# Kernel optimization log

Hardware: AMD Instinct MI355X
Metric: run time of the kernel (lower is better)

Reference implementation:

```python
import jax, jax.numpy as jnp
import numpy as np
from jax import lax

HFACTOR = 0.5


def setup_inputs() -> dict:
    key = jax.random.key(0)
    ks = jax.random.split(key, 10)
    B, T, D, K, C = 256, 128, 768, 74, 128
    feats = jax.random.normal(ks[0], (B, T, D), jnp.float32)
    attention_mask = jnp.ones((B, T), jnp.int32)
    labels = jax.random.randint(ks[1], (B, T), 0, K)
    cache = jax.random.normal(ks[2], (C, 128, K), jnp.float32)
    W1 = jax.random.normal(ks[3], (D, K), jnp.float32) * 0.02
    b1 = jnp.zeros((K,), jnp.float32)
    W2 = jax.random.normal(ks[4], (K, K), jnp.float32) * 0.1
    b2 = jnp.zeros((K,), jnp.float32)
    start_trans = jax.random.normal(ks[5], (K,), jnp.float32) * 0.1
    end_trans = jax.random.normal(ks[6], (K,), jnp.float32) * 0.1
    transitions = jax.random.normal(ks[7], (K, K), jnp.float32) * 0.1
    return dict(feats=feats, attention_mask=attention_mask, labels=labels,
                cache=cache, W1=W1, b1=b1, W2=W2, b2=b2,
                start_trans=start_trans, end_trans=end_trans,
                transitions=transitions)


def _crf_normalizer(em, mask, start, end, trans):
    # em: [T,B,K], mask: [T,B] bool -> log partition per batch [B]
    score0 = start[None, :] + em[0]
    def step(score, inp):
        e, m = inp
        nxt = jax.nn.logsumexp(score[:, :, None] + trans[None] + e[:, None, :], axis=1)
        return jnp.where(m[:, None], nxt, score), None
    score, _ = lax.scan(step, score0, (em[1:], mask[1:]))
    return jax.nn.logsumexp(score + end[None, :], axis=1)


def _crf_score(em, tags, mask, start, end, trans):
    # em: [T,B,K], tags: [T,B], mask: [T,B] -> gold path score [B]
    T, B, K = em.shape
    b = jnp.arange(B)
    score0 = start[tags[0]] + em[0, b, tags[0]]
    maskf = mask.astype(em.dtype)
    def step(carry, inp):
        score, prev = carry
        e, t, m = inp
        score = score + (trans[prev, t] + e[b, t]) * m
        return (score, t), None
    (score, _), _ = lax.scan(step, (score0, tags[0]), (em[1:], tags[1:], maskf[1:]))
    seq_ends = jnp.sum(mask.astype(jnp.int32), axis=0) - 1  # [B]
    last = tags[seq_ends, b]
    return score + end[last]


def _viterbi(em, mask, start, end, trans):
    # em: [T,B,K], mask: [T,B] bool -> best tag sequence [B,T]
    T, B, K = em.shape
    b = jnp.arange(B)
    score0 = start[None, :] + em[0]
    def fwd(score, inp):
        e, m = inp
        br = score[:, :, None] + trans[None]          # [B,K_prev,K_cur]
        idx = jnp.argmax(br, axis=1)                  # [B,K]
        nxt = jnp.max(br, axis=1) + e
        return jnp.where(m[:, None], nxt, score), idx
    score, hist = lax.scan(fwd, score0, (em[1:], mask[1:]))  # hist: [T-1,B,K]
    best_last = jnp.argmax(score + end[None, :], axis=1)     # [B]
    def back(cur, inp):
        h, m = inp                                    # h: [B,K], m: [B]
        cur_t = jnp.where(m, h[b, cur], best_last)
        return cur_t, cur_t
    _, tags_rev = lax.scan(back, best_last, (hist[::-1], mask[1:][::-1]))
    tags = jnp.concatenate([tags_rev[::-1], best_last[None]], axis=0)  # [T,B]
    return tags.T


def reference(feats, attention_mask, labels, cache, W1, b1, W2, b2,
              start_trans, end_trans, transitions):
    T = feats.shape[1]
    logits = feats @ W1 + b1                                   # [B,T,K]
    c = cache[:, :T]                                           # [C,T,K]
    sim = jnp.einsum('pjk,qjk->pq', logits, c)                 # [B,C]
    p = jax.nn.softmax(sim, axis=1)
    h = jnp.einsum('ij,jkl->ikl', p, c)                        # [B,T,K]
    new_logits = (logits + h * HFACTOR) @ W2 + b2              # [B,T,K]
    em = jnp.transpose(new_logits, (1, 0, 2))                  # [T,B,K]
    mask_t = attention_mask.T.astype(bool)                     # [T,B]
    prob = _viterbi(em, mask_t, start_trans, end_trans, transitions)
    num = _crf_score(em, labels.T, mask_t, start_trans, end_trans, transitions)
    den = _crf_normalizer(em, mask_t, start_trans, end_trans, transitions)
    loss = -jnp.mean(num - den)                                # torchcrf reduction='mean', negated
    return (prob, loss)
```

## Files before the change

### kernel.cpp

```cpp
#include <hip/hip_runtime.h>

#define B_ 256
#define T_ 128
#define D_ 768
#define K_ 74
#define C_ 128
#define TK_ 9472
#define BT_ 32768
#define EMS_ 18944

#define LGKM_BARRIER() do { \
    asm volatile("s_waitcnt lgkmcnt(0)" ::: "memory"); \
    __builtin_amdgcn_s_barrier(); \
    __builtin_amdgcn_sched_barrier(0); \
} while (0)

__global__ void pad_weights(const float* __restrict__ W1, const float* __restrict__ W2,
                            float* __restrict__ W1q, float* __restrict__ W2q)
{
    int idx = blockIdx.x * 256 + threadIdx.x;
    if (idx < 4 * 768 * 20) {
        int nq = idx / (768 * 20); int rem = idx - nq * (768 * 20);
        int k = rem / 20, j = rem - k * 20;
        int c = nq * 19 + j;
        W1q[idx] = (j < 19 && c < 74) ? W1[k * 74 + c] : 0.f;
    }
    if (idx < 4 * 74 * 20) {
        int nq = idx / (74 * 20); int rem = idx - nq * (74 * 20);
        int k = rem / 20, j = rem - k * 20;
        int c = nq * 19 + j;
        W2q[idx] = (j < 19 && c < 74) ? W2[k * 74 + c] : 0.f;
    }
}

__global__ __launch_bounds__(256) void gemm_logits(const float* __restrict__ feats,
    const float* __restrict__ W1q, const float* __restrict__ b1, float* __restrict__ logits)
{
    int orig = blockIdx.x;
    int vb = (orig & 7) * 64 + (orig >> 3);
    int rb = vb >> 2, nq = vb & 3;
    int tid = threadIdx.x;
    int r = rb * 256 + tid;
    int c0 = nq * 19;
    const float* frow = feats + (size_t)r * 768;
    const float* wq = W1q + nq * (768 * 20);
    float acc[20];
    #pragma unroll
    for (int j = 0; j < 20; ++j) acc[j] = 0.f;

    for (int k0 = 0; k0 < 768; k0 += 16) {
        float4 a[4];
        #pragma unroll
        for (int q = 0; q < 4; ++q) a[q] = *(const float4*)(frow + k0 + 4 * q);
        #pragma unroll
        for (int u = 0; u < 16; ++u) {
            float av = ((const float*)a)[u];
            const float* wr = wq + (k0 + u) * 20;
            #pragma unroll
            for (int j = 0; j < 20; ++j) acc[j] += av * wr[j];
        }
    }
    #pragma unroll
    for (int j = 0; j < 19; ++j) {
        int c = c0 + j;
        if (c < 74) logits[(size_t)r * 74 + c] = acc[j] + b1[c];
    }
}

__global__ __launch_bounds__(256) void sim_partial(const float* __restrict__ logits,
    const float* __restrict__ cache, float* __restrict__ part)
{
    __shared__ float As[74][68];
    __shared__ float Bs[74][68];
    int tid = threadIdx.x;
    int tx = tid & 15, ty = tid >> 4;
    int bid = blockIdx.x;
    int jc = bid >> 3;
    int mt = (bid >> 1) & 3;
    int nt = bid & 1;
    int p0 = mt * 64, q0 = nt * 64;
    float acc[4][4] = {};
    for (int jj = 0; jj < 4; ++jj) {
        int j = jc * 4 + jj;
        for (int it = 0; it < 19; ++it) {
            int lin = it * 256 + tid;
            if (lin < 64 * 74) {
                int r = lin / 74, ik = lin - r * 74;
                As[ik][r] = logits[(p0 + r) * TK_ + j * 74 + ik];
                Bs[ik][r] = cache[(q0 + r) * TK_ + j * 74 + ik];
            }
        }
        __syncthreads();
        for (int ik = 0; ik < 74; ++ik) {
            float4 a = *(const float4*)&As[ik][4 * tx];
            float4 b = *(const float4*)&Bs[ik][4 * ty];
            const float* ap = (const float*)&a;
            const float* bp = (const float*)&b;
            #pragma unroll
            for (int i = 0; i < 4; ++i)
                #pragma unroll
                for (int q = 0; q < 4; ++q) acc[i][q] += ap[i] * bp[q];
        }
        __syncthreads();
    }
    #pragma unroll
    for (int i = 0; i < 4; ++i)
        #pragma unroll
        for (int q = 0; q < 4; ++q)
            part[jc * (B_ * C_) + (p0 + 4 * tx + i) * C_ + q0 + 4 * ty + q] = acc[i][q];
}

__global__ void sim_reduce(const float* __restrict__ part, float* __restrict__ sim)
{
    int idx = blockIdx.x * 256 + threadIdx.x;
    float s = 0.f;
    for (int jc = 0; jc < 32; ++jc) s += part[jc * (B_ * C_) + idx];
    sim[idx] = s;
}

__global__ void softmax128(const float* __restrict__ sim, float* __restrict__ p)
{
    __shared__ float red[128];
    int q = threadIdx.x, row = blockIdx.x;
    float v = sim[row * 128 + q];
    red[q] = v; __syncthreads();
    for (int s = 64; s > 0; s >>= 1) { if (q < s) red[q] = fmaxf(red[q], red[q + s]); __syncthreads(); }
    float m = red[0]; __syncthreads();
    float e = expf(v - m);
    red[q] = e; __syncthreads();
    for (int s = 64; s > 0; s >>= 1) { if (q < s) red[q] += red[q + s]; __syncthreads(); }
    float sum = red[0];
    p[row * 128 + q] = e / sum;
}

__global__ __launch_bounds__(256) void gemm_h_y(const float* __restrict__ pmat,
    const float* __restrict__ cache, const float* __restrict__ logits, float* __restrict__ y)
{
    __shared__ float As[128][68];
    __shared__ float Bs[128][68];
    int tid = threadIdx.x;
    int tx = tid & 15, ty = tid >> 4;
    int mt = blockIdx.x / 148, nt = blockIdx.x - mt * 148;
    int r0 = mt * 64, n0 = nt * 64;
    #pragma unroll
    for (int it = 0; it < 32; ++it) {
        int lin = it * 256 + tid;
        int r = lin >> 7, kk = lin & 127;
        As[kk][r] = pmat[(r0 + r) * 128 + kk];
    }
    #pragma unroll
    for (int it = 0; it < 32; ++it) {
        int lin = it * 256 + tid;
        int kk = lin >> 6, c = lin & 63;
        Bs[kk][c] = cache[kk * TK_ + n0 + c];
    }
    __syncthreads();
    float acc[4][4] = {};
    for (int kk = 0; kk < 128; ++kk) {
        float4 a = *(const float4*)&As[kk][4 * tx];
        float4 b = *(const float4*)&Bs[kk][4 * ty];
        const float* ap = (const float*)&a;
        const float* bp = (const float*)&b;
        #pragma unroll
        for (int i = 0; i < 4; ++i)
            #pragma unroll
            for (int j = 0; j < 4; ++j) acc[i][j] += ap[i] * bp[j];
    }
    #pragma unroll
    for (int i = 0; i < 4; ++i) {
        int r = r0 + 4 * tx + i;
        #pragma unroll
        for (int j = 0; j < 4; ++j) {
            int n = n0 + 4 * ty + j;
            y[r * TK_ + n] = logits[r * TK_ + n] + 0.5f * acc[i][j];
        }
    }
}

__global__ __launch_bounds__(256) void gemm_em(const float* __restrict__ y,
    const float* __restrict__ W2q, const float* __restrict__ b2, float* __restrict__ em)
{
    int orig = blockIdx.x;
    int vb = (orig & 7) * 64 + (orig >> 3);
    int rb = vb >> 2, nq = vb & 3;
    int tid = threadIdx.x;
    int r = rb * 256 + tid;
    int c0 = nq * 19;
    const float* wq = W2q + nq * (74 * 20);
    const float* yrow = y + (size_t)r * 74;
    float acc[20];
    #pragma unroll
    for (int j = 0; j < 20; ++j) acc[j] = 0.f;
    #pragma unroll 1
    for (int k0 = 0; k0 < 74; k0 += 2) {
        float2 a = *(const float2*)(yrow + k0);
        const float* ap = (const float*)&a;
        #pragma unroll
        for (int u = 0; u < 2; ++u) {
            const float* wr = wq + (k0 + u) * 20;
            #pragma unroll
            for (int j = 0; j < 20; ++j) acc[j] += ap[u] * wr[j];
        }
    }
    int b = r >> 7, t = r & 127;
    #pragma unroll
    for (int j = 0; j < 19; ++j) {
        int c = c0 + j;
        if (c < 74) em[t * EMS_ + b * 74 + c] = acc[j] + b2[c];
    }
}

__global__ __launch_bounds__(256) void crf_scan(const float* __restrict__ em,
    const int* __restrict__ mask_, const float* __restrict__ startv,
    const float* __restrict__ endv, const float* __restrict__ trans,
    float* __restrict__ out_tags, float* __restrict__ den)
{
    __shared__ float transS[74 * 74];
    __shared__ float scoreS[2][88];
    __shared__ float EscS[88] __attribute__((aligned(16)));
    __shared__ float pv[3][74];
    __shared__ int   pi[3][74];
    __shared__ unsigned char histS[127 * 74];
    __shared__ float tagsS[128];
    __shared__ float Ms[2];
    __shared__ int   flagU[2];
    __shared__ int   maskS[128];
    int tid = threadIdx.x;
    bool isV = blockIdx.x < 256;
    int b = isV ? blockIdx.x : (blockIdx.x - 256);

    for (int i = tid; i < 74 * 74; i += 256) transS[i] = trans[i];
    if (tid < 128) maskS[tid] = mask_[b * 128 + tid];
    if (tid >= 74 && tid < 88) { scoreS[0][tid] = -3.0e38f; scoreS[1][tid] = -3.0e38f; EscS[tid] = 0.f; }
    if (tid < 74) scoreS[0][tid] = startv[tid] + em[b * 74 + tid];
    __syncthreads();

    int ch = (tid < 74) ? 0 : (tid < 148 ? 1 : 2);
    int kp = tid - ch * 74;
    int cbase = ch * 28;
    float tr[28];
    if (tid < 222) {
        #pragma unroll
        for (int j = 0; j < 28; ++j) {
            int kk = cbase + j;
            tr[j] = (kk < 74) ? transS[kk * 74 + kp] : -1.0e30f;
        }
    }
    int cur = 0;

    float eA = 0.f, eB = 0.f;
    if (tid < 74) {
        eA = em[1 * EMS_ + b * 74 + tid];
        eB = em[2 * EMS_ + b * 74 + tid];
    }

    if (isV) {
        for (int t = 1; t < 128; ++t) {
            float eC = 0.f;
            if (tid < 74 && t + 2 < 128) eC = em[(t + 2) * EMS_ + b * 74 + tid];
            if (tid < 222) {
                float m = -3.0e38f; int mi = cbase;
                #pragma unroll
                for (int jj = 0; jj < 7; ++jj) {
                    float4 s4 = *(const float4*)&scoreS[cur][cbase + 4 * jj];
                    const float* sp = (const float*)&s4;
                    #pragma unroll
                    for (int u = 0; u < 4; ++u) {
                        float v = sp[u] + tr[4 * jj + u];
                        if (v > m) { m = v; mi = cbase + 4 * jj + u; }
                    }
                }
                pv[ch][kp] = m; pi[ch][kp] = mi;
            }
            LGKM_BARRIER();
            int mk = maskS[t];
            if (tid < 74) {
                float m0 = pv[0][tid]; int i0 = pi[0][tid];
                if (pv[1][tid] > m0) { m0 = pv[1][tid]; i0 = pi[1][tid]; }
                if (pv[2][tid] > m0) { m0 = pv[2][tid]; i0 = pi[2][tid]; }
                histS[(t - 1) * 74 + tid] = (unsigned char)i0;
                scoreS[cur ^ 1][tid] = mk ? (m0 + eA) : scoreS[cur][tid];
            }
            LGKM_BARRIER();
            cur ^= 1;
            eA = eB; eB = eC;
        }
        if (tid == 0) {
            float bm = scoreS[cur][0] + endv[0]; int bi = 0;
            for (int k = 1; k < 74; ++k) {
                float v = scoreS[cur][k] + endv[k];
                if (v > bm) { bm = v; bi = k; }
            }
            int curk = bi;
            tagsS[127] = (float)bi;
            for (int ti = 126; ti >= 0; --ti) {
                int mk = maskS[ti + 1];
                curk = mk ? (int)histS[ti * 74 + curk] : bi;
                tagsS[ti] = (float)curk;
            }
        }
        __syncthreads();
        if (tid < 128) out_tags[b * 128 + tid] = tagsS[tid];
    } else {
        if (tid < 222) {
            #pragma unroll
            for (int j = 0; j < 28; ++j) tr[j] = __expf(tr[j]);
        }
        float v0 = (tid < 74) ? scoreS[0][tid] : -3.0e38f;
        float M;
        if (tid < 128) {
            #pragma unroll
            for (int off = 32; off > 0; off >>= 1) v0 = fmaxf(v0, __shfl_xor(v0, off));
            if ((tid & 63) == 0) Ms[tid >> 6] = v0;
        }
        __syncthreads();
        M = fmaxf(Ms[0], Ms[1]);
        if (tid < 74) EscS[tid] = __expf(scoreS[0][tid] - M);
        LGKM_BARRIER();
        for (int t = 1; t < 128; ++t) {
            float eC = 0.f;
            if (tid < 74 && t + 2 < 128) eC = em[(t + 2) * EMS_ + b * 74 + tid];
            if (tid < 222) {
                float s0 = 0.f, s1 = 0.f, s2 = 0.f, s3 = 0.f;
                #pragma unroll
                for (int jj = 0; jj < 7; ++jj) {
                    float4 E4 = *(const float4*)&EscS[cbase + 4 * jj];
                    s0 += E4.x * tr[4 * jj + 0];
                    s1 += E4.y * tr[4 * jj + 1];
                    s2 += E4.z * tr[4 * jj + 2];
                    s3 += E4.w * tr[4 * jj + 3];
                }
                pv[ch][kp] = (s0 + s1) + (s2 + s3);
            }
            LGKM_BARRIER();
            int mk = maskS[t];
            int over = 0, notunder = 0;
            float snew = 0.f;
            if (tid < 74) {
                float sum = pv[0][tid] + pv[1][tid] + pv[2][tid];
                float nxt = M + __logf(sum) + eA;
                snew = mk ? nxt : scoreS[cur][tid];
                scoreS[cur ^ 1][tid] = snew;
                EscS[tid] = __expf(snew - M);
                over = (snew > M + 55.0f) ? 1 : 0;
                notunder = (snew >= M - 40.0f) ? 1 : 0;
            }
            int refresh = __any(over) | (!__any(notunder));
            if ((tid & 63) == 0 && tid < 128) flagU[tid >> 6] = refresh;
            LGKM_BARRIER();
            cur ^= 1;
            if (flagU[0] | flagU[1]) {
                float v = (tid < 74) ? scoreS[cur][tid] : -3.0e38f;
                if (tid < 128) {
                    #pragma unroll
                    for (int off = 32; off > 0; off >>= 1) v = fmaxf(v, __shfl_xor(v, off));
                    if ((tid & 63) == 0) Ms[tid >> 6] = v;
                }
                LGKM_BARRIER();
                M = fmaxf(Ms[0], Ms[1]);
                if (tid < 74) EscS[tid] = __expf(scoreS[cur][tid] - M);
                LGKM_BARRIER();
            }
            eA = eB; eB = eC;
        }
        if (tid == 0) {
            float m = -3.0e38f;
            for (int k = 0; k < 74; ++k) m = fmaxf(m, scoreS[cur][k] + endv[k]);
            float s = 0.f;
            for (int k = 0; k < 74; ++k) s += __expf(scoreS[cur][k] + endv[k] - m);
            den[b] = m + __logf(s);
        }
    }
}

__global__ __launch_bounds__(128) void loss_partial(const float* __restrict__ em,
    const int* __restrict__ labels, const int* __restrict__ mask_,
    const float* __restrict__ startv, const float* __restrict__ endv,
    const float* __restrict__ den, const float* __restrict__ trans, float* __restrict__ nd)
{
    __shared__ float cs[2];
    __shared__ int ms[2];
    int b = blockIdx.x, t = threadIdx.x;
    int lab = labels[b * 128 + t];
    int mk = mask_[b * 128 + t];
    float contrib;
    if (t == 0) {
        contrib = startv[lab] + em[b * 74 + lab];
    } else {
        int labp = labels[b * 128 + t - 1];
        contrib = mk ? (trans[labp * 74 + lab] + em[t * EMS_ + b * 74 + lab]) : 0.f;
    }
    float c = contrib; int m = mk;
    #pragma unroll
    for (int off = 32; off > 0; off >>= 1) {
        c += __shfl_xor(c, off);
        m += __shfl_xor(m, off);
    }
    if ((t & 63) == 0) { cs[t >> 6] = c; ms[t >> 6] = m; }
    __syncthreads();
    if (t == 0) {
        float num = cs[0] + cs[1];
        int msum = ms[0] + ms[1];
        int last = labels[b * 128 + msum - 1];
        num += endv[last];
        nd[b] = num - den[b];
    }
}

__global__ void loss_final(const float* __restrict__ nd, float* __restrict__ out_loss)
{
    __shared__ float red[256];
    int i = threadIdx.x;
    red[i] = nd[i];
    __syncthreads();
    for (int s = 128; s > 0; s >>= 1) { if (i < s) red[i] += red[i + s]; __syncthreads(); }
    if (i == 0) out_loss[0] = -(red[0] / 256.f);
}

extern "C" void kernel_launch(void* const* d_in, const int* in_sizes, int n_in,
                              void* d_out, int out_size, void* d_ws, size_t ws_size,
                              hipStream_t stream)
{
    const float* feats  = (const float*)d_in[0];
    const int*   amask  = (const int*)d_in[1];
    const int*   labels = (const int*)d_in[2];
    const float* cache  = (const float*)d_in[3];
    const float* W1     = (const float*)d_in[4];
    const float* b1     = (const float*)d_in[5];
    const float* W2     = (const float*)d_in[6];
    const float* b2     = (const float*)d_in[7];
    const float* startv = (const float*)d_in[8];
    const float* endv   = (const float*)d_in[9];
    const float* trans  = (const float*)d_in[10];

    float* ws     = (float*)d_ws;
    float* logits = ws;
    float* y      = ws + 2424832;
    float* em     = ws + 4849664;
    float* part   = ws + 7274496;
    float* sim    = ws + 8323072;
    float* p      = ws + 8355840;
    float* den    = ws + 8388608;
    float* nd     = ws + 8388864;
    float* W1q    = ws + 8389120;
    float* W2q    = ws + 8450560;
    float* out_tags = (float*)d_out;
    float* out_loss = (float*)d_out + 32768;

    hipLaunchKernelGGL(pad_weights,  dim3(240), dim3(256), 0, stream, W1, W2, W1q, W2q);
    hipLaunchKernelGGL(gemm_logits,  dim3(512), dim3(256), 0, stream, feats, W1q, b1, logits);
    hipLaunchKernelGGL(sim_partial,  dim3(256), dim3(256), 0, stream, logits, cache, part);
    hipLaunchKernelGGL(sim_reduce,   dim3(128), dim3(256), 0, stream, part, sim);
    hipLaunchKernelGGL(softmax128,   dim3(256), dim3(128), 0, stream, sim, p);
    hipLaunchKernelGGL(gemm_h_y,     dim3(592), dim3(256), 0, stream, p, cache, logits, y);
    hipLaunchKernelGGL(gemm_em,      dim3(512), dim3(256), 0, stream, y, W2q, b2, em);
    hipLaunchKernelGGL(crf_scan,     dim3(512), dim3(256), 0, stream, em, amask, startv, endv, trans, out_tags, den);
    hipLaunchKernelGGL(loss_partial, dim3(256), dim3(128), 0, stream, em, labels, amask, startv, endv, den, trans, nd);
    hipLaunchKernelGGL(loss_final,   dim3(1),   dim3(256), 0, stream, nd, out_loss);
}
```

Baseline: 302.0 us.

## Split logits GEMM over K halves and collapse CRF scan to one barrier per step

The feature-projection GEMM is split into two K halves, doubling the block count to 1024. A separate elementwise kernel then sums the two partial outputs and adds the bias. The CRF Viterbi and forward scans now give each of 74 threads the full 76-wide transition column in registers, which removes the three-way partial reduction and one barrier per time step. The forward scan double-buffers the exp-score array. The trade-offs are fewer active threads per step, higher register pressure from the 76-float array, and an extra kernel launch plus a read-modify-write pass over the logits.

```diff
diff --git a/kernel.cpp b/kernel.cpp
--- a/kernel.cpp
+++ b/kernel.cpp
@@ -33,22 +33,22 @@
     }
 }
 
-__global__ __launch_bounds__(256) void gemm_logits(const float* __restrict__ feats,
-    const float* __restrict__ W1q, const float* __restrict__ b1, float* __restrict__ logits)
+__global__ __launch_bounds__(256) void gemm_logits_part(const float* __restrict__ feats,
+    const float* __restrict__ W1q, float* __restrict__ outA, float* __restrict__ outB)
 {
     int orig = blockIdx.x;
-    int vb = (orig & 7) * 64 + (orig >> 3);
-    int rb = vb >> 2, nq = vb & 3;
+    int vb = (orig & 7) * 128 + (orig >> 3);
+    int rb = vb >> 3, nq = (vb >> 1) & 3, ks = vb & 1;
     int tid = threadIdx.x;
     int r = rb * 256 + tid;
     int c0 = nq * 19;
-    const float* frow = feats + (size_t)r * 768;
-    const float* wq = W1q + nq * (768 * 20);
+    const float* frow = feats + (size_t)r * 768 + ks * 384;
+    const float* wq = W1q + nq * (768 * 20) + ks * 384 * 20;
     float acc[20];
     #pragma unroll
     for (int j = 0; j < 20; ++j) acc[j] = 0.f;
 
-    for (int k0 = 0; k0 < 768; k0 += 16) {
+    for (int k0 = 0; k0 < 384; k0 += 16) {
         float4 a[4];
         #pragma unroll
         for (int q = 0; q < 4; ++q) a[q] = *(const float4*)(frow + k0 + 4 * q);
@@ -60,11 +60,20 @@
             for (int j = 0; j < 20; ++j) acc[j] += av * wr[j];
         }
     }
+    float* P = ks ? outB : outA;
     #pragma unroll
     for (int j = 0; j < 19; ++j) {
         int c = c0 + j;
-        if (c < 74) logits[(size_t)r * 74 + c] = acc[j] + b1[c];
-    }
+        if (c < 74) P[(size_t)r * 74 + c] = acc[j];
+    }
+}
+
+__global__ void logits_sum(const float* __restrict__ Bp, const float* __restrict__ b1,
+                           float* __restrict__ logits)
+{
+    int idx = blockIdx.x * 256 + threadIdx.x;
+    int r = idx / 74; int c = idx - r * 74;
+    logits[idx] = logits[idx] + Bp[idx] + b1[c];
 }
 
 __global__ __launch_bounds__(256) void sim_partial(const float* __restrict__ logits,
@@ -216,10 +225,8 @@
     float* __restrict__ out_tags, float* __restrict__ den)
 {
     __shared__ float transS[74 * 74];
-    __shared__ float scoreS[2][88];
-    __shared__ float EscS[88] __attribute__((aligned(16)));
-    __shared__ float pv[3][74];
-    __shared__ int   pi[3][74];
+    __shared__ float scoreS[2][76] __attribute__((aligned(16)));
+    __shared__ float EscS[2][76] __attribute__((aligned(16)));
     __shared__ unsigned char histS[127 * 74];
     __shared__ float tagsS[128];
     __shared__ float Ms[2];
@@ -231,20 +238,17 @@
 
     for (int i = tid; i < 74 * 74; i += 256) transS[i] = trans[i];
     if (tid < 128) maskS[tid] = mask_[b * 128 + tid];
-    if (tid >= 74 && tid < 88) { scoreS[0][tid] = -3.0e38f; scoreS[1][tid] = -3.0e38f; EscS[tid] = 0.f; }
+    if (tid >= 74 && tid < 76) {
+        scoreS[0][tid] = -3.0e38f; scoreS[1][tid] = -3.0e38f;
+        EscS[0][tid] = 0.f;        EscS[1][tid] = 0.f;
+    }
     if (tid < 74) scoreS[0][tid] = startv[tid] + em[b * 74 + tid];
     __syncthreads();
 
-    int ch = (tid < 74) ? 0 : (tid < 148 ? 1 : 2);
-    int kp = tid - ch * 74;
-    int cbase = ch * 28;
-    float tr[28];
-    if (tid < 222) {
-        #pragma unroll
-        for (int j = 0; j < 28; ++j) {
-            int kk = cbase + j;
-            tr[j] = (kk < 74) ? transS[kk * 74 + kp] : -1.0e30f;
-        }
+    float tr[76];
+    if (tid < 74) {
+        #pragma unroll
+        for (int k = 0; k < 76; ++k) tr[k] = (k < 74) ? transS[k * 74 + tid] : -1.0e30f;
     }
     int cur = 0;
 
@@ -258,28 +262,22 @@
         for (int t = 1; t < 128; ++t) {
             float eC = 0.f;
             if (tid < 74 && t + 2 < 128) eC = em[(t + 2) * EMS_ + b * 74 + tid];
-            if (tid < 222) {
-                float m = -3.0e38f; int mi = cbase;
+            if (tid < 74) {
+                float m = -3.0e38f; int mi = 0;
                 #pragma unroll
-                for (int jj = 0; jj < 7; ++jj) {
-                    float4 s4 = *(const float4*)&scoreS[cur][cbase + 4 * jj];
+                for (int kk = 0; kk < 19; ++kk) {
+                    float4 s4 = *(const float4*)&scoreS[cur][4 * kk];
                     const float* sp = (const float*)&s4;
                     #pragma unroll
                     for (int u = 0; u < 4; ++u) {
-                        float v = sp[u] + tr[4 * jj + u];
-                        if (v > m) { m = v; mi = cbase + 4 * jj + u; }
+                        float v = sp[u] + tr[4 * kk + u];
+                        if (v > m) { m = v; mi = 4 * kk + u; }
                     }
                 }
-                pv[ch][kp] = m; pi[ch][kp] = mi;
-            }
-            LGKM_BARRIER();
-            int mk = maskS[t];
-            if (tid < 74) {
-                float m0 = pv[0][tid]; int i0 = pi[0][tid];
-                if (pv[1][tid] > m0) { m0 = pv[1][tid]; i0 = pi[1][tid]; }
-                if (pv[2][tid] > m0) { m0 = pv[2][tid]; i0 = pi[2][tid]; }
-                histS[(t - 1) * 74 + tid] = (unsigned char)i0;
-                scoreS[cur ^ 1][tid] = mk ? (m0 + eA) : scoreS[cur][tid];
+                float sown = scoreS[cur][tid];
+                histS[(t - 1) * 74 + tid] = (unsigned char)mi;
+                int mk = maskS[t];
+                scoreS[cur ^ 1][tid] = mk ? (m + eA) : sown;
             }
             LGKM_BARRIER();
             cur ^= 1;
@@ -302,9 +300,9 @@
         __syncthreads();
         if (tid < 128) out_tags[b * 128 + tid] = tagsS[tid];
     } else {
-        if (tid < 222) {
-            #pragma unroll
-            for (int j = 0; j < 28; ++j) tr[j] = __expf(tr[j]);
+        if (tid < 74) {
+            #pragma unroll
+            for (int k = 0; k < 76; ++k) tr[k] = __expf(tr[k]);
         }
         float v0 = (tid < 74) ? scoreS[0][tid] : -3.0e38f;
         float M;
@@ -315,33 +313,29 @@
         }
         __syncthreads();
         M = fmaxf(Ms[0], Ms[1]);
-        if (tid < 74) EscS[tid] = __expf(scoreS[0][tid] - M);
+        if (tid < 74) EscS[0][tid] = __expf(scoreS[0][tid] - M);
         LGKM_BARRIER();
         for (int t = 1; t < 128; ++t) {
             float eC = 0.f;
             if (tid < 74 && t + 2 < 128) eC = em[(t + 2) * EMS_ + b * 74 + tid];
-            if (tid < 222) {
+            int over = 0, notunder = 0;
+            if (tid < 74) {
                 float s0 = 0.f, s1 = 0.f, s2 = 0.f, s3 = 0.f;
                 #pragma unroll
-                for (int jj = 0; jj < 7; ++jj) {
-                    float4 E4 = *(const float4*)&EscS[cbase + 4 * jj];
-                    s0 += E4.x * tr[4 * jj + 0];
-                    s1 += E4.y * tr[4 * jj + 1];
-                    s2 += E4.z * tr[4 * jj + 2];
-                    s3 += E4.w * tr[4 * jj + 3];
+                for (int kk = 0; kk < 19; ++kk) {
+                    float4 E4 = *(const float4*)&EscS[cur][4 * kk];
+                    s0 += E4.x * tr[4 * kk + 0];
+                    s1 += E4.y * tr[4 * kk + 1];
+                    s2 += E4.z * tr[4 * kk + 2];
+                    s3 += E4.w * tr[4 * kk + 3];
                 }
-                pv[ch][kp] = (s0 + s1) + (s2 + s3);
-            }
-            LGKM_BARRIER();
-            int mk = maskS[t];
-            int over = 0, notunder = 0;
-            float snew = 0.f;
-            if (tid < 74) {
-                float sum = pv[0][tid] + pv[1][tid] + pv[2][tid];
+                float sum = (s0 + s1) + (s2 + s3);
+                float sown = scoreS[cur][tid];
                 float nxt = M + __logf(sum) + eA;
-                snew = mk ? nxt : scoreS[cur][tid];
+                int mk = maskS[t];
+                float snew = mk ? nxt : sown;
                 scoreS[cur ^ 1][tid] = snew;
-                EscS[tid] = __expf(snew - M);
+                EscS[cur ^ 1][tid] = __expf(snew - M);
                 over = (snew > M + 55.0f) ? 1 : 0;
                 notunder = (snew >= M - 40.0f) ? 1 : 0;
             }
@@ -358,7 +352,7 @@
                 }
                 LGKM_BARRIER();
                 M = fmaxf(Ms[0], Ms[1]);
-                if (tid < 74) EscS[tid] = __expf(scoreS[cur][tid] - M);
+                if (tid < 74) EscS[cur][tid] = __expf(scoreS[cur][tid] - M);
                 LGKM_BARRIER();
             }
             eA = eB; eB = eC;
@@ -442,19 +436,20 @@
     float* p      = ws + 8355840;
     float* den    = ws + 8388608;
     float* nd     = ws + 8388864;
-    float* W1q    = ws + 8389120;
-    float* W2q    = ws + 8450560;
+    float* W2q    = ws + 8389120;
+    float* W1q    = part;
     float* out_tags = (float*)d_out;
     float* out_loss = (float*)d_out + 32768;
 
-    hipLaunchKernelGGL(pad_weights,  dim3(240), dim3(256), 0, stream, W1, W2, W1q, W2q);
-    hipLaunchKernelGGL(gemm_logits,  dim3(512), dim3(256), 0, stream, feats, W1q, b1, logits);
-    hipLaunchKernelGGL(sim_partial,  dim3(256), dim3(256), 0, stream, logits, cache, part);
-    hipLaunchKernelGGL(sim_reduce,   dim3(128), dim3(256), 0, stream, part, sim);
-    hipLaunchKernelGGL(softmax128,   dim3(256), dim3(128), 0, stream, sim, p);
-    hipLaunchKernelGGL(gemm_h_y,     dim3(592), dim3(256), 0, stream, p, cache, logits, y);
-    hipLaunchKernelGGL(gemm_em,      dim3(512), dim3(256), 0, stream, y, W2q, b2, em);
-    hipLaunchKernelGGL(crf_scan,     dim3(512), dim3(256), 0, stream, em, amask, startv, endv, trans, out_tags, den);
-    hipLaunchKernelGGL(loss_partial, dim3(256), dim3(128), 0, stream, em, labels, amask, startv, endv, den, trans, nd);
-    hipLaunchKernelGGL(loss_final,   dim3(1),   dim3(256), 0, stream, nd, out_loss);
-}
+    hipLaunchKernelGGL(pad_weights,      dim3(240),  dim3(256), 0, stream, W1, W2, W1q, W2q);
+    hipLaunchKernelGGL(gemm_logits_part, dim3(1024), dim3(256), 0, stream, feats, W1q, logits, y);
+    hipLaunchKernelGGL(logits_sum,       dim3(9472), dim3(256), 0, stream, y, b1, logits);
+    hipLaunchKernelGGL(sim_partial,      dim3(256),  dim3(256), 0, stream, logits, cache, part);
+    hipLaunchKernelGGL(sim_reduce,       dim3(128),  dim3(256), 0, stream, part, sim);
+    hipLaunchKernelGGL(softmax128,       dim3(256),  dim3(128), 0, stream, sim, p);
+    hipLaunchKernelGGL(gemm_h_y,         dim3(592),  dim3(256), 0, stream, p, cache, logits, y);
+    hipLaunchKernelGGL(gemm_em,          dim3(512),  dim3(256), 0, stream, y, W2q, b2, em);
+    hipLaunchKernelGGL(crf_scan,         dim3(512),  dim3(256), 0, stream, em, amask, startv, endv, trans, out_tags, den);
+    hipLaunchKernelGGL(loss_partial,     dim3(256),  dim3(128), 0, stream, em, labels, amask, startv, endv, den, trans, nd);
+    hipLaunchKernelGGL(loss_final,       dim3(1),    dim3(256), 0, stream, nd, out_loss);
+}
```

Measured after the change: 333.6 us. 1.1x slower.
